# Kernel tuning notes

Hardware: AMD Instinct MI355X
Metric: run time of the kernel (lower is better)

## Reference

```python
import jax, jax.numpy as jnp
import numpy as np
from jax import lax

N_CHANNELS = 16
FIRE_RATE = 0.5
STEP_SIZE = 1.0
ALPHA_THRESH = 0.1

_identity = np.array([[0.0, 0.0, 0.0], [0.0, 1.0, 0.0], [0.0, 0.0, 0.0]], np.float32)
_dx = np.array([[-0.125, 0.0, 0.125], [-0.25, 0.0, 0.25], [-0.125, 0.0, 0.125]], np.float32)
_dy = _dx.T
# angle = 0.0 -> cos=1, sin=0 -> filters unchanged
_all_filters = np.stack((_identity, _dx, _dy))              # (3,3,3)
_filters = np.tile(_all_filters, (N_CHANNELS, 1, 1))[:, None]  # (48,1,3,3) OIHW
PERCEIVE_FILTERS = jnp.asarray(_filters)


def wrap_edges(x):
    # circular pad of 1 on H and W; x: [B,C,H,W]
    return jnp.pad(x, ((0, 0), (0, 0), (1, 1), (1, 1)), mode='wrap')


def living_mask(x):
    alpha = x[:, 3:4]                                   # [B,1,H,W]
    pooled = lax.reduce_window(wrap_edges(alpha), -jnp.inf, lax.max,
                               (1, 1, 3, 3), (1, 1, 1, 1), 'VALID')
    return pooled > ALPHA_THRESH                        # [B,1,H,W] bool


def perceive(x):
    # depthwise 3x3 with 3 filters per channel, circular boundary
    return lax.conv_general_dilated(
        wrap_edges(x), PERCEIVE_FILTERS,
        window_strides=(1, 1), padding='VALID',
        dimension_numbers=('NCHW', 'OIHW', 'NCHW'),
        feature_group_count=N_CHANNELS)                 # [B,48,H,W]


def setup_inputs() -> dict:
    key = jax.random.key(0)
    k1, k2, k3, k4 = jax.random.split(key, 4)
    B, C, H, W = 16, N_CHANNELS, 256, 256
    x = jax.random.uniform(k1, (B, C, H, W), dtype=jnp.float32)
    rand_vals = jax.random.uniform(k2, (B, 1, H, W), dtype=jnp.float32)
    w1 = jax.random.normal(k3, (3 * C, 128), dtype=jnp.float32) * 0.05
    b1 = jnp.zeros((128,), jnp.float32)
    w2 = jax.random.normal(k4, (128, 16), dtype=jnp.float32) * 0.05
    b2 = jnp.zeros((16,), jnp.float32)
    return {"x": x, "rand_vals": rand_vals, "w1": w1, "b1": b1, "w2": w2, "b2": b2}


def reference(x, rand_vals, w1, b1, w2, b2):
    pre_life = living_mask(x)
    p = perceive(x)                                      # [B,48,H,W]
    h = jax.nn.relu(jnp.einsum('bchw,cd->bdhw', p, w1) + b1[None, :, None, None])
    dx = (jnp.einsum('bchw,cd->bdhw', h, w2) + b2[None, :, None, None]) * STEP_SIZE
    update_mask = (rand_vals < FIRE_RATE).astype(x.dtype)  # [B,1,H,W]
    x = x + dx * update_mask
    post_life = living_mask(x)
    life = (pre_life & post_life).astype(x.dtype)
    return x * life
```

## Files before the change

### kernel.cpp

```cpp
#include <hip/hip_runtime.h>
#include <hip/hip_bf16.h>

typedef __attribute__((ext_vector_type(8))) short bf16x8;
typedef __attribute__((ext_vector_type(4))) short bf16x4;
typedef __attribute__((ext_vector_type(4))) float f32x4;
typedef __attribute__((ext_vector_type(4))) unsigned int u32x4;
typedef __attribute__((ext_vector_type(2))) unsigned int u32x2;

#define NC   16
#define IMG  (256*256)

#define P_STRIDE  112
#define W1_OFF    28672
#define W1_STRIDE 112
#define W2_OFF    43008
#define B1_OFF    47360
#define B2_OFF    47872
#define LDS_TOT   47936
#define BNC_SZ    9472
#define BNC_DX    4352

static __device__ __forceinline__ unsigned short f2bf(float f) {
    union { __hip_bfloat16 h; unsigned short u; } cv;
    cv.h = __float2bfloat16(f);
    return cv.u;
}
static __device__ __forceinline__ unsigned int packbf2(float a, float b) {
    return (unsigned int)f2bf(a) | ((unsigned int)f2bf(b) << 16);
}
static __device__ __forceinline__ f32x4 mfma_bf16_16x16x16(bf16x4 a, bf16x4 b, f32x4 c) {
#if __has_builtin(__builtin_amdgcn_mfma_f32_16x16x16bf16_1k)
    return __builtin_amdgcn_mfma_f32_16x16x16bf16_1k(a, b, c, 0, 0, 0);
#else
    f32x4 d;
    asm("v_mfma_f32_16x16x16_bf16 %0, %1, %2, %3" : "=v"(d) : "v"(a), "v"(b), "v"(c));
    return d;
#endif
}

__global__ __launch_bounds__(256, 3) void nca_update_mfma(
    const float* __restrict__ x, const float* __restrict__ rand_vals,
    const float* __restrict__ w1, const float* __restrict__ b1,
    const float* __restrict__ w2, const float* __restrict__ b2,
    float* __restrict__ out, float* __restrict__ alpha_ws)
{
    __shared__ __align__(16) unsigned char lds[LDS_TOT];
    const int t = threadIdx.x;

    const int wg = (blockIdx.x & 7) * 512 + (blockIdx.x >> 3);
    const int b  = wg >> 8;
    const int h  = wg & 255;
    const int w  = t;

    #pragma unroll
    for (int i = 0; i < 24; i++) {
        int idx = i*256 + t;
        int n = idx & 127, k = idx >> 7;
        *(unsigned short*)(lds + W1_OFF + n*W1_STRIDE + k*2) = f2bf(w1[k*128 + n]);
    }
    #pragma unroll
    for (int i = 0; i < 8; i++) {
        int idx = i*256 + t;
        int c = idx & 15, k = idx >> 4;
        *(unsigned short*)(lds + W2_OFF + c*272 + k*2) = f2bf(w2[k*16 + c]);
    }
    if (t < 128) *(float*)(lds + B1_OFF + t*4) = b1[t];
    if (t < 16)  *(float*)(lds + B2_OFF + t*4) = b2[t];

    const int hm = (h + 255) & 255, hp = (h + 1) & 255;
    const int wm = (w + 255) & 255, wp = (w + 1) & 255;
    const float* xb = x + (size_t)b * NC * IMG;
    const int r0o = hm*256, r1o = h*256, r2o = hp*256;

    const float rv = rand_vals[b*IMG + r1o + w];

    float buf[2][18];
    unsigned int pk[24];
    float xc[16];
    float premax = 0.0f;

    #pragma unroll
    for (int cc = 0; cc < 2; cc++) {
        const float* xc_ = xb + cc*IMG;
        float* bu = &buf[0][cc*9];
        bu[0]=xc_[r0o+wm]; bu[1]=xc_[r0o+w]; bu[2]=xc_[r0o+wp];
        bu[3]=xc_[r1o+wm]; bu[4]=xc_[r1o+w]; bu[5]=xc_[r1o+wp];
        bu[6]=xc_[r2o+wm]; bu[7]=xc_[r2o+w]; bu[8]=xc_[r2o+wp];
    }
    #pragma unroll
    for (int pr = 0; pr < 8; pr++) {
        if (pr < 7) {
            #pragma unroll
            for (int cc = 0; cc < 2; cc++) {
                const float* xc_ = xb + ((pr+1)*2 + cc)*IMG;
                float* bu = &buf[(pr+1)&1][cc*9];
                bu[0]=xc_[r0o+wm]; bu[1]=xc_[r0o+w]; bu[2]=xc_[r0o+wp];
                bu[3]=xc_[r1o+wm]; bu[4]=xc_[r1o+w]; bu[5]=xc_[r1o+wp];
                bu[6]=xc_[r2o+wm]; bu[7]=xc_[r2o+w]; bu[8]=xc_[r2o+wp];
            }
        }
        float pv[6];
        #pragma unroll
        for (int cc = 0; cc < 2; cc++) {
            const float* a = &buf[pr&1][cc*9];
            pv[cc*3+0] = a[4];
            xc[pr*2+cc] = a[4];
            pv[cc*3+1] = 0.125f*(a[2]-a[0]) + 0.25f*(a[5]-a[3]) + 0.125f*(a[8]-a[6]);
            pv[cc*3+2] = 0.125f*(a[6]-a[0]) + 0.25f*(a[7]-a[1]) + 0.125f*(a[8]-a[2]);
            if (pr*2 + cc == 3)
                premax = fmaxf(fmaxf(fmaxf(a[0],a[1]),fmaxf(a[2],a[3])),
                         fmaxf(fmaxf(a[4],a[5]),fmaxf(fmaxf(a[6],a[7]),a[8])));
        }
        pk[pr*3+0] = packbf2(pv[0], pv[1]);
        pk[pr*3+1] = packbf2(pv[2], pv[3]);
        pk[pr*3+2] = packbf2(pv[4], pv[5]);
    }

    {
        u32x4* pvv = (u32x4*)(lds + t*P_STRIDE);
        #pragma unroll
        for (int j = 0; j < 6; j++) {
            u32x4 v = {pk[4*j], pk[4*j+1], pk[4*j+2], pk[4*j+3]};
            pvv[j] = v;
        }
    }
    __syncthreads();

    const int wv = t >> 6, l15 = t & 15, lg = (t >> 4) & 3;

    bf16x8 A1a[8]; bf16x4 A1b[8];
    #pragma unroll
    for (int mt = 0; mt < 8; mt++) {
        const unsigned char* r = lds + W1_OFF + (mt*16 + l15)*W1_STRIDE;
        A1a[mt] = *(const bf16x8*)(r + lg*16);
        A1b[mt] = *(const bf16x4*)(r + 64 + lg*8);
    }
    bf16x8 Bpa[4]; bf16x4 Bpb[4];
    #pragma unroll
    for (int pt = 0; pt < 4; pt++) {
        const unsigned char* r = lds + (wv*64 + pt*16 + l15)*P_STRIDE;
        Bpa[pt] = *(const bf16x8*)(r + lg*16);
        Bpb[pt] = *(const bf16x4*)(r + 64 + lg*8);
    }
    bf16x8 A2[4];
    #pragma unroll
    for (int kt = 0; kt < 4; kt++)
        A2[kt] = *(const bf16x8*)(lds + W2_OFF + l15*272 + kt*64 + lg*16);
    f32x4 b2frag = *(const f32x4*)(lds + B2_OFF + lg*16);

    asm volatile("s_waitcnt lgkmcnt(0)" ::: "memory");
    __builtin_amdgcn_sched_barrier(0);
    __syncthreads();

    unsigned char* hb  = lds + wv*BNC_SZ;
    unsigned char* dxb = lds + wv*BNC_SZ + BNC_DX;

    #pragma unroll
    for (int pt = 0; pt < 4; pt++) {
        f32x4 hacc[8];
        __builtin_amdgcn_s_setprio(1);
        #pragma unroll
        for (int mt = 0; mt < 8; mt++) {
            f32x4 a = *(const f32x4*)(lds + B1_OFF + (mt*16 + lg*4)*4);
            a = __builtin_amdgcn_mfma_f32_16x16x32_bf16(A1a[mt], Bpa[pt], a, 0,0,0);
            a = mfma_bf16_16x16x16(A1b[mt], Bpb[pt], a);
            hacc[mt] = a;
        }
        __builtin_amdgcn_s_setprio(0);
        asm volatile("s_waitcnt lgkmcnt(0)" ::: "memory");
        __builtin_amdgcn_sched_barrier(0);
        #pragma unroll
        for (int mt = 0; mt < 8; mt++) {
            u32x2 pk2 = {packbf2(fmaxf(hacc[mt][0],0.f), fmaxf(hacc[mt][1],0.f)),
                         packbf2(fmaxf(hacc[mt][2],0.f), fmaxf(hacc[mt][3],0.f))};
            *(u32x2*)(hb + l15*272 + mt*32 + lg*8) = pk2;
        }
        asm volatile("s_waitcnt lgkmcnt(0)" ::: "memory");
        __builtin_amdgcn_sched_barrier(0);
        f32x4 acc2 = b2frag;
        __builtin_amdgcn_s_setprio(1);
        #pragma unroll
        for (int kt = 0; kt < 4; kt++) {
            bf16x8 Bh = *(const bf16x8*)(hb + l15*272 + kt*64 + lg*16);
            acc2 = __builtin_amdgcn_mfma_f32_16x16x32_bf16(A2[kt], Bh, acc2, 0,0,0);
        }
        __builtin_amdgcn_s_setprio(0);
        *(f32x4*)(dxb + (pt*16 + l15)*80 + lg*16) = acc2;
    }
    asm volatile("s_waitcnt lgkmcnt(0)" ::: "memory");
    __builtin_amdgcn_sched_barrier(0);

    const unsigned char* myd = lds + wv*BNC_SZ + BNC_DX + (t & 63)*80;
    float dxv[16];
    *(f32x4*)&dxv[0]  = *(const f32x4*)(myd +  0);
    *(f32x4*)&dxv[4]  = *(const f32x4*)(myd + 16);
    *(f32x4*)&dxv[8]  = *(const f32x4*)(myd + 32);
    *(f32x4*)&dxv[12] = *(const f32x4*)(myd + 48);

    const float fm    = (rv < 0.5f)     ? 1.0f : 0.0f;
    const float lifep = (premax > 0.1f) ? 1.0f : 0.0f;

    alpha_ws[b*IMG + r1o + w] = fmaf(dxv[3], fm, xc[3]);

    float* ob = out + (size_t)b*NC*IMG + r1o + w;
    #pragma unroll
    for (int c = 0; c < 16; c++)
        ob[(size_t)c*IMG] = fmaf(dxv[c], fm, xc[c]) * lifep;
}

__global__ __launch_bounds__(256) void nca_postmask(
    const float* __restrict__ alpha_ws, float* __restrict__ out)
{
    const int wg = (blockIdx.x & 7) * 512 + (blockIdx.x >> 3);
    const int b  = wg >> 8;
    const int h  = wg & 255;
    const int w  = threadIdx.x;
    const int hm = (h + 255) & 255, hp = (h + 1) & 255;
    const int wm = (w + 255) & 255, wp = (w + 1) & 255;

    const float* na = alpha_ws + b*IMG;
    const float* n0 = na + hm*256;
    const float* n1 = na + h *256;
    const float* n2 = na + hp*256;
    float post = fmaxf(fmaxf(fmaxf(n0[wm],n0[w]),fmaxf(n0[wp],n1[wm])),
                 fmaxf(fmaxf(n1[w],n1[wp]),fmaxf(fmaxf(n2[wm],n2[w]),n2[wp])));
    if (!(post > 0.1f)) {
        float* ob = out + (size_t)b*NC*IMG + h*256 + w;
        #pragma unroll
        for (int c = 0; c < 16; c++) ob[c*IMG] = 0.0f;
    }
}

extern "C" void kernel_launch(void* const* d_in, const int* in_sizes, int n_in,
                              void* d_out, int out_size, void* d_ws, size_t ws_size,
                              hipStream_t stream) {
    const float* x         = (const float*)d_in[0];
    const float* rand_vals = (const float*)d_in[1];
    const float* w1        = (const float*)d_in[2];
    const float* b1        = (const float*)d_in[3];
    const float* w2        = (const float*)d_in[4];
    const float* b2        = (const float*)d_in[5];
    float* out      = (float*)d_out;
    float* alpha_ws = (float*)d_ws;

    const int grid = 16 * 256;
    nca_update_mfma<<<grid, 256, 0, stream>>>(x, rand_vals, w1, b1, w2, b2,
                                              out, alpha_ws);
    nca_postmask<<<grid, 256, 0, stream>>>(alpha_ws, out);
}
```

Baseline: 61.83 us.

## Process four rows per workgroup to amortize weight staging

Each workgroup of the update kernel now handles four consecutive image rows instead of one, so the grid shrinks by four. The W1/W2/bias conversion into LDS and the register loading of weight fragments happen once and are reused across the rows, which removes per-block setup cost. In exchange there is less parallelism, extra barriers per row, and the perceive loads for the next row are not overlapped with the MFMA work.

```diff
diff --git a/kernel.cpp b/kernel.cpp
--- a/kernel.cpp
+++ b/kernel.cpp
@@ -9,6 +9,7 @@
 
 #define NC   16
 #define IMG  (256*256)
+#define ROWS 4
 
 #define P_STRIDE  112
 #define W1_OFF    28672
@@ -46,11 +47,14 @@
 {
     __shared__ __align__(16) unsigned char lds[LDS_TOT];
     const int t = threadIdx.x;
-
-    const int wg = (blockIdx.x & 7) * 512 + (blockIdx.x >> 3);
-    const int b  = wg >> 8;
-    const int h  = wg & 255;
+    const int wv = t >> 6, l15 = t & 15, lg = (t >> 4) & 3;
+
+    const int wg = (blockIdx.x & 7) * 128 + (blockIdx.x >> 3);
+    const int b  = wg >> 6;
+    const int h0 = (wg & 63) * ROWS;
     const int w  = t;
+    const int wm = (w + 255) & 255, wp = (w + 1) & 255;
+    const float* xb = x + (size_t)b * NC * IMG;
 
     #pragma unroll
     for (int i = 0; i < 24; i++) {
@@ -67,66 +71,65 @@
     if (t < 128) *(float*)(lds + B1_OFF + t*4) = b1[t];
     if (t < 16)  *(float*)(lds + B2_OFF + t*4) = b2[t];
 
-    const int hm = (h + 255) & 255, hp = (h + 1) & 255;
-    const int wm = (w + 255) & 255, wp = (w + 1) & 255;
-    const float* xb = x + (size_t)b * NC * IMG;
-    const int r0o = hm*256, r1o = h*256, r2o = hp*256;
-
-    const float rv = rand_vals[b*IMG + r1o + w];
-
     float buf[2][18];
     unsigned int pk[24];
     float xc[16];
-    float premax = 0.0f;
-
-    #pragma unroll
-    for (int cc = 0; cc < 2; cc++) {
-        const float* xc_ = xb + cc*IMG;
-        float* bu = &buf[0][cc*9];
-        bu[0]=xc_[r0o+wm]; bu[1]=xc_[r0o+w]; bu[2]=xc_[r0o+wp];
-        bu[3]=xc_[r1o+wm]; bu[4]=xc_[r1o+w]; bu[5]=xc_[r1o+wp];
-        bu[6]=xc_[r2o+wm]; bu[7]=xc_[r2o+w]; bu[8]=xc_[r2o+wp];
-    }
-    #pragma unroll
-    for (int pr = 0; pr < 8; pr++) {
-        if (pr < 7) {
+    float premax, rv;
+
+    auto perceive = [&](int hh) {
+        const int hm = (hh + 255) & 255, hp = (hh + 1) & 255;
+        const int r0o = hm*256, r1c = hh*256, r2o = hp*256;
+        rv = rand_vals[b*IMG + r1c + w];
+        premax = 0.0f;
+        #pragma unroll
+        for (int cc = 0; cc < 2; cc++) {
+            const float* xc_ = xb + cc*IMG;
+            float* bu = &buf[0][cc*9];
+            bu[0]=xc_[r0o+wm]; bu[1]=xc_[r0o+w]; bu[2]=xc_[r0o+wp];
+            bu[3]=xc_[r1c+wm]; bu[4]=xc_[r1c+w]; bu[5]=xc_[r1c+wp];
+            bu[6]=xc_[r2o+wm]; bu[7]=xc_[r2o+w]; bu[8]=xc_[r2o+wp];
+        }
+        #pragma unroll
+        for (int pr = 0; pr < 8; pr++) {
+            if (pr < 7) {
+                #pragma unroll
+                for (int cc = 0; cc < 2; cc++) {
+                    const float* xc_ = xb + ((pr+1)*2 + cc)*IMG;
+                    float* bu = &buf[(pr+1)&1][cc*9];
+                    bu[0]=xc_[r0o+wm]; bu[1]=xc_[r0o+w]; bu[2]=xc_[r0o+wp];
+                    bu[3]=xc_[r1c+wm]; bu[4]=xc_[r1c+w]; bu[5]=xc_[r1c+wp];
+                    bu[6]=xc_[r2o+wm]; bu[7]=xc_[r2o+w]; bu[8]=xc_[r2o+wp];
+                }
+            }
+            float pv[6];
             #pragma unroll
             for (int cc = 0; cc < 2; cc++) {
-                const float* xc_ = xb + ((pr+1)*2 + cc)*IMG;
-                float* bu = &buf[(pr+1)&1][cc*9];
-                bu[0]=xc_[r0o+wm]; bu[1]=xc_[r0o+w]; bu[2]=xc_[r0o+wp];
-                bu[3]=xc_[r1o+wm]; bu[4]=xc_[r1o+w]; bu[5]=xc_[r1o+wp];
-                bu[6]=xc_[r2o+wm]; bu[7]=xc_[r2o+w]; bu[8]=xc_[r2o+wp];
-            }
-        }
-        float pv[6];
-        #pragma unroll
-        for (int cc = 0; cc < 2; cc++) {
-            const float* a = &buf[pr&1][cc*9];
-            pv[cc*3+0] = a[4];
-            xc[pr*2+cc] = a[4];
-            pv[cc*3+1] = 0.125f*(a[2]-a[0]) + 0.25f*(a[5]-a[3]) + 0.125f*(a[8]-a[6]);
-            pv[cc*3+2] = 0.125f*(a[6]-a[0]) + 0.25f*(a[7]-a[1]) + 0.125f*(a[8]-a[2]);
-            if (pr*2 + cc == 3)
-                premax = fmaxf(fmaxf(fmaxf(a[0],a[1]),fmaxf(a[2],a[3])),
-                         fmaxf(fmaxf(a[4],a[5]),fmaxf(fmaxf(a[6],a[7]),a[8])));
-        }
-        pk[pr*3+0] = packbf2(pv[0], pv[1]);
-        pk[pr*3+1] = packbf2(pv[2], pv[3]);
-        pk[pr*3+2] = packbf2(pv[4], pv[5]);
-    }
-
-    {
+                const float* a = &buf[pr&1][cc*9];
+                pv[cc*3+0] = a[4];
+                xc[pr*2+cc] = a[4];
+                pv[cc*3+1] = 0.125f*(a[2]-a[0]) + 0.25f*(a[5]-a[3]) + 0.125f*(a[8]-a[6]);
+                pv[cc*3+2] = 0.125f*(a[6]-a[0]) + 0.25f*(a[7]-a[1]) + 0.125f*(a[8]-a[2]);
+                if (pr*2 + cc == 3)
+                    premax = fmaxf(fmaxf(fmaxf(a[0],a[1]),fmaxf(a[2],a[3])),
+                             fmaxf(fmaxf(a[4],a[5]),fmaxf(fmaxf(a[6],a[7]),a[8])));
+            }
+            pk[pr*3+0] = packbf2(pv[0], pv[1]);
+            pk[pr*3+1] = packbf2(pv[2], pv[3]);
+            pk[pr*3+2] = packbf2(pv[4], pv[5]);
+        }
+    };
+    auto stage_p = [&]() {
         u32x4* pvv = (u32x4*)(lds + t*P_STRIDE);
         #pragma unroll
         for (int j = 0; j < 6; j++) {
             u32x4 v = {pk[4*j], pk[4*j+1], pk[4*j+2], pk[4*j+3]};
             pvv[j] = v;
         }
-    }
+    };
+
+    perceive(h0);
+    stage_p();
     __syncthreads();
-
-    const int wv = t >> 6, l15 = t & 15, lg = (t >> 4) & 3;
 
     bf16x8 A1a[8]; bf16x4 A1b[8];
     #pragma unroll
@@ -155,57 +158,81 @@
     unsigned char* hb  = lds + wv*BNC_SZ;
     unsigned char* dxb = lds + wv*BNC_SZ + BNC_DX;
 
-    #pragma unroll
-    for (int pt = 0; pt < 4; pt++) {
-        f32x4 hacc[8];
-        __builtin_amdgcn_s_setprio(1);
-        #pragma unroll
-        for (int mt = 0; mt < 8; mt++) {
-            f32x4 a = *(const f32x4*)(lds + B1_OFF + (mt*16 + lg*4)*4);
-            a = __builtin_amdgcn_mfma_f32_16x16x32_bf16(A1a[mt], Bpa[pt], a, 0,0,0);
-            a = mfma_bf16_16x16x16(A1b[mt], Bpb[pt], a);
-            hacc[mt] = a;
-        }
-        __builtin_amdgcn_s_setprio(0);
+    int h = h0;
+    #pragma unroll 1
+    for (int row = 0; row < ROWS; ++row) {
+        #pragma unroll
+        for (int pt = 0; pt < 4; pt++) {
+            f32x4 hacc[8];
+            __builtin_amdgcn_s_setprio(1);
+            #pragma unroll
+            for (int mt = 0; mt < 8; mt++) {
+                f32x4 a = *(const f32x4*)(lds + B1_OFF + (mt*16 + lg*4)*4);
+                a = __builtin_amdgcn_mfma_f32_16x16x32_bf16(A1a[mt], Bpa[pt], a, 0,0,0);
+                a = mfma_bf16_16x16x16(A1b[mt], Bpb[pt], a);
+                hacc[mt] = a;
+            }
+            __builtin_amdgcn_s_setprio(0);
+            asm volatile("s_waitcnt lgkmcnt(0)" ::: "memory");
+            __builtin_amdgcn_sched_barrier(0);
+            #pragma unroll
+            for (int mt = 0; mt < 8; mt++) {
+                u32x2 pk2 = {packbf2(fmaxf(hacc[mt][0],0.f), fmaxf(hacc[mt][1],0.f)),
+                             packbf2(fmaxf(hacc[mt][2],0.f), fmaxf(hacc[mt][3],0.f))};
+                *(u32x2*)(hb + l15*272 + mt*32 + lg*8) = pk2;
+            }
+            asm volatile("s_waitcnt lgkmcnt(0)" ::: "memory");
+            __builtin_amdgcn_sched_barrier(0);
+            f32x4 acc2 = b2frag;
+            __builtin_amdgcn_s_setprio(1);
+            #pragma unroll
+            for (int kt = 0; kt < 4; kt++) {
+                bf16x8 Bh = *(const bf16x8*)(hb + l15*272 + kt*64 + lg*16);
+                acc2 = __builtin_amdgcn_mfma_f32_16x16x32_bf16(A2[kt], Bh, acc2, 0,0,0);
+            }
+            __builtin_amdgcn_s_setprio(0);
+            *(f32x4*)(dxb + (pt*16 + l15)*80 + lg*16) = acc2;
+        }
         asm volatile("s_waitcnt lgkmcnt(0)" ::: "memory");
         __builtin_amdgcn_sched_barrier(0);
-        #pragma unroll
-        for (int mt = 0; mt < 8; mt++) {
-            u32x2 pk2 = {packbf2(fmaxf(hacc[mt][0],0.f), fmaxf(hacc[mt][1],0.f)),
-                         packbf2(fmaxf(hacc[mt][2],0.f), fmaxf(hacc[mt][3],0.f))};
-            *(u32x2*)(hb + l15*272 + mt*32 + lg*8) = pk2;
-        }
-        asm volatile("s_waitcnt lgkmcnt(0)" ::: "memory");
-        __builtin_amdgcn_sched_barrier(0);
-        f32x4 acc2 = b2frag;
-        __builtin_amdgcn_s_setprio(1);
-        #pragma unroll
-        for (int kt = 0; kt < 4; kt++) {
-            bf16x8 Bh = *(const bf16x8*)(hb + l15*272 + kt*64 + lg*16);
-            acc2 = __builtin_amdgcn_mfma_f32_16x16x32_bf16(A2[kt], Bh, acc2, 0,0,0);
-        }
-        __builtin_amdgcn_s_setprio(0);
-        *(f32x4*)(dxb + (pt*16 + l15)*80 + lg*16) = acc2;
-    }
-    asm volatile("s_waitcnt lgkmcnt(0)" ::: "memory");
-    __builtin_amdgcn_sched_barrier(0);
-
-    const unsigned char* myd = lds + wv*BNC_SZ + BNC_DX + (t & 63)*80;
-    float dxv[16];
-    *(f32x4*)&dxv[0]  = *(const f32x4*)(myd +  0);
-    *(f32x4*)&dxv[4]  = *(const f32x4*)(myd + 16);
-    *(f32x4*)&dxv[8]  = *(const f32x4*)(myd + 32);
-    *(f32x4*)&dxv[12] = *(const f32x4*)(myd + 48);
-
-    const float fm    = (rv < 0.5f)     ? 1.0f : 0.0f;
-    const float lifep = (premax > 0.1f) ? 1.0f : 0.0f;
-
-    alpha_ws[b*IMG + r1o + w] = fmaf(dxv[3], fm, xc[3]);
-
-    float* ob = out + (size_t)b*NC*IMG + r1o + w;
-    #pragma unroll
-    for (int c = 0; c < 16; c++)
-        ob[(size_t)c*IMG] = fmaf(dxv[c], fm, xc[c]) * lifep;
+
+        {
+            const int r1o = h*256;
+            const unsigned char* myd = dxb + (t & 63)*80;
+            float dxv[16];
+            *(f32x4*)&dxv[0]  = *(const f32x4*)(myd +  0);
+            *(f32x4*)&dxv[4]  = *(const f32x4*)(myd + 16);
+            *(f32x4*)&dxv[8]  = *(const f32x4*)(myd + 32);
+            *(f32x4*)&dxv[12] = *(const f32x4*)(myd + 48);
+
+            const float fm    = (rv < 0.5f)     ? 1.0f : 0.0f;
+            const float lifep = (premax > 0.1f) ? 1.0f : 0.0f;
+
+            alpha_ws[b*IMG + r1o + w] = fmaf(dxv[3], fm, xc[3]);
+
+            float* ob = out + (size_t)b*NC*IMG + r1o + w;
+            #pragma unroll
+            for (int c = 0; c < 16; c++)
+                ob[(size_t)c*IMG] = fmaf(dxv[c], fm, xc[c]) * lifep;
+        }
+
+        if (row < ROWS - 1) {
+            perceive(h + 1);
+            h = h + 1;
+            __syncthreads();
+            stage_p();
+            __syncthreads();
+            #pragma unroll
+            for (int pt = 0; pt < 4; pt++) {
+                const unsigned char* r = lds + (wv*64 + pt*16 + l15)*P_STRIDE;
+                Bpa[pt] = *(const bf16x8*)(r + lg*16);
+                Bpb[pt] = *(const bf16x4*)(r + 64 + lg*8);
+            }
+            asm volatile("s_waitcnt lgkmcnt(0)" ::: "memory");
+            __builtin_amdgcn_sched_barrier(0);
+            __syncthreads();
+        }
+    }
 }
 
 __global__ __launch_bounds__(256) void nca_postmask(
@@ -243,8 +270,7 @@
     float* out      = (float*)d_out;
     float* alpha_ws = (float*)d_ws;
 
-    const int grid = 16 * 256;
-    nca_update_mfma<<<grid, 256, 0, stream>>>(x, rand_vals, w1, b1, w2, b2,
-                                              out, alpha_ws);
-    nca_postmask<<<grid, 256, 0, stream>>>(alpha_ws, out);
-}
+    nca_update_mfma<<<16*256/ROWS, 256, 0, stream>>>(x, rand_vals, w1, b1, w2, b2,
+                                                     out, alpha_ws);
+    nca_postmask<<<16*256, 256, 0, stream>>>(alpha_ws, out);
+}
```

Result: slower. 66.95 us (+8.3%).
